# Optimization experiments

Measured on AMD Instinct MI355X. Metric: run time of the kernel, lower is better.

Reference implementation:

```python
import jax, jax.numpy as jnp
import numpy as np

D_MODEL = 1024
N_HEADS = 16
HEAD = D_MODEL // N_HEADS
B, S = 2, 2048


def setup_inputs() -> dict:
    key = jax.random.key(0)
    ks = jax.random.split(key, 9)
    sc = 1.0 / np.sqrt(D_MODEL)
    return {
        "q": jax.random.normal(ks[0], (B, S, D_MODEL), dtype=jnp.float32),
        "k": jax.random.normal(ks[1], (B, S, D_MODEL), dtype=jnp.float32),
        "v": jax.random.normal(ks[2], (B, S, D_MODEL), dtype=jnp.float32),
        "mask": jnp.zeros((S, S), dtype=jnp.float32),
        "Wq": jax.random.normal(ks[3], (D_MODEL, D_MODEL), dtype=jnp.float32) * sc,
        "bq": jnp.zeros((D_MODEL,), dtype=jnp.float32),
        "Wk": jax.random.normal(ks[4], (D_MODEL, D_MODEL), dtype=jnp.float32) * sc,
        "bk": jnp.zeros((D_MODEL,), dtype=jnp.float32),
        "Wv": jax.random.normal(ks[5], (D_MODEL, D_MODEL), dtype=jnp.float32) * sc,
        "bv": jnpp_zeros() if False else jnp.zeros((D_MODEL,), dtype=jnp.float32),
    }


def reference(q, k, v, mask, Wq, bq, Wk, bk, Wv, bv):
    # Linear projections (torch Linear: x @ W.T + b)
    qp = q @ Wq.T + bq  # (B, S, D)
    kp = k @ Wk.T + bk
    vp = v @ Wv.T + bv
    # split heads -> (B, H, S, Hd)
    def split(x):
        return x.reshape(B, S, N_HEADS, HEAD).transpose(0, 2, 1, 3)
    qh, kh, vh = split(qp), split(kp), split(vp)
    scores = jnp.einsum('bhqd,bhkd->bhqk', qh, kh) / np.sqrt(HEAD)
    scores = scores + mask  # additive mask broadcast over (B, H)
    attn = jax.nn.softmax(scores, axis=-1)
    out = jnp.einsum('bhqk,bhkd->bhqd', attn, vh)
    return out.transpose(0, 2, 1, 3).reshape(B, S, D_MODEL)
```

## Files before the change

### kernel.cpp

```cpp
#include <hip/hip_runtime.h>
#include <cstdint>

#define DM 1024
#define NH 16
#define HDIM 64
#define SEQ 2048
#define NB 2
#define L2E 1.44269504f

typedef unsigned short u16;
typedef unsigned int u32;
typedef __attribute__((ext_vector_type(8))) short bf16x8;
typedef __attribute__((ext_vector_type(8))) unsigned short u16x8;
typedef __attribute__((ext_vector_type(4))) unsigned int u32x4;
typedef __attribute__((ext_vector_type(4))) float f32x4;
typedef __attribute__((ext_vector_type(16))) float f32x16;
typedef __attribute__((ext_vector_type(4))) unsigned short u16x4;

__device__ __forceinline__ u16 f2bf(float f) {
  uint32_t x = __float_as_uint(f);
  x += 0x7fffu + ((x >> 16) & 1u);
  return (u16)(x >> 16);
}

__device__ __forceinline__ u32 pack_bf2t(float lo, float hi) {
  return __builtin_amdgcn_perm(__float_as_uint(hi), __float_as_uint(lo), 0x07060302u);
}

__device__ __forceinline__ void gload_lds16(const void* g, void* lds) {
  __builtin_amdgcn_global_load_lds(
      (const __attribute__((address_space(1))) unsigned int*)(uintptr_t)g,
      (__attribute__((address_space(3))) unsigned int*)(uint32_t)(uintptr_t)lds,
      16, 0, 0);
}


__global__ __launch_bounds__(256) void prep_kernel(
    const float4* __restrict__ W0, const float4* __restrict__ W1, const float4* __restrict__ W2,
    u16x4* __restrict__ d0, u16x4* __restrict__ d1, u16x4* __restrict__ d2,
    const float* __restrict__ mask, u16* __restrict__ maskP) {
  const int bx = blockIdx.x;
  const int t = threadIdx.x;
  if (bx < 3072) {
    const int i = bx * 256 + t;
    const int seg = i >> 18, off = i & 262143;
    const float4* s = seg == 0 ? W0 : (seg == 1 ? W1 : W2);
    u16x4* d = seg == 0 ? d0 : (seg == 1 ? d1 : d2);
    float4 v = s[off];
    u16x4 o = {f2bf(v.x), f2bf(v.y), f2bf(v.z), f2bf(v.w)};
    d[off] = o;
    return;
  }
  __shared__ float tile[32][257];
  const int mb = bx - 3072;
  const int q0 = (mb & 63) * 32;
  const int yt = mb >> 6;
#pragma unroll
  for (int ss = 0; ss < 2; ++ss) {
    const int st = yt * 2 + ss;
    const int kv0 = st * 256;
    if (ss) __syncthreads();
#pragma unroll
    for (int p = 0; p < 8; ++p) {
      const int row = p * 4 + (t >> 6);
      const int col = (t & 63) * 4;
      *(float4*)&tile[row][col] = *(const float4*)&mask[(size_t)(q0 + row) * SEQ + kv0 + col];
    }
    __syncthreads();
    const int tgl = t >> 5, ql = t & 31;
    u16 outv[32];
#pragma unroll
    for (int i = 0; i < 32; ++i) {
      const int hl = i >> 4, r = i & 15;
      const int kvl = (r & 3) + 8 * (r >> 2) + 4 * hl;
      outv[i] = f2bf(tile[ql][tgl * 32 + kvl] * L2E);
    }
    u16* dst = maskP + ((size_t)(st * 8 + tgl) * SEQ + (q0 + ql)) * 32;
#pragma unroll
    for (int j = 0; j < 4; ++j) *(u16x8*)(dst + 8 * j) = *(const u16x8*)&outv[8 * j];
  }
}

__global__ __launch_bounds__(256) void proj_kernel(
    const float* __restrict__ Xq, const float* __restrict__ Xk, const float* __restrict__ Xv,
    const u16* __restrict__ Wqp, const u16* __restrict__ Wkp, const u16* __restrict__ Wvp,
    const float* __restrict__ bqp, const float* __restrict__ bkp, const float* __restrict__ bvp,
    u16* __restrict__ Qp, u16* __restrict__ Kp, u16* __restrict__ Vt) {
  __shared__ __align__(16) u16 sA[2][128 * 32];
  __shared__ __align__(16) u16 sB[2][128 * 32];
  const int t = threadIdx.x;
  const int w = t >> 6, lane = t & 63, quad = lane >> 4, l16 = lane & 15;
  const int wr = w >> 1, wc = w & 1;
  const int m0 = blockIdx.y * 128, n0 = blockIdx.x * 128;
  const int mode = blockIdx.z;
  const float* X = mode == 0 ? Xq : (mode == 1 ? Xk : Xv);
  const u16* W = mode == 0 ? Wqp : (mode == 1 ? Wkp : Wvp);
  const float* bias = mode == 0 ? bqp : (mode == 1 ? bkp : bvp);

  f32x4 acc[4][4] = {};
  const int ar = t >> 3;
  const int ac = t & 7;
  const int srow = lane >> 2;
  const int scol = (lane & 3) * 16;

  {
    float4 x0[4];
#pragma unroll
    for (int rr = 0; rr < 4; ++rr)
      x0[rr] = *(const float4*)&X[(size_t)(m0 + rr * 32 + ar) * DM + ac * 4];
#pragma unroll
    for (int rr = 0; rr < 4; ++rr) {
      u16x4 pk = {f2bf(x0[rr].x), f2bf(x0[rr].y), f2bf(x0[rr].z), f2bf(x0[rr].w)};
      *(u16x4*)&sA[0][(rr * 32 + ar) * 32 + ac * 4] = pk;
    }
#pragma unroll
    for (int j = 0; j < 2; ++j) {
      const int rbase = (w * 2 + j) * 16;
      gload_lds16((const char*)W + ((size_t)(n0 + rbase + srow) * DM) * 2 + scol,
                  (char*)sB[0] + rbase * 64);
    }
  }

  for (int it = 0; it < 32; ++it) {
    const int p = it & 1;
    __syncthreads();
    float4 xn[4];
    if (it < 31) {
      const int k0 = (it + 1) * 32;
#pragma unroll
      for (int rr = 0; rr < 4; ++rr)
        xn[rr] = *(const float4*)&X[(size_t)(m0 + rr * 32 + ar) * DM + k0 + ac * 4];
#pragma unroll
      for (int j = 0; j < 2; ++j) {
        const int rbase = (w * 2 + j) * 16;
        gload_lds16((const char*)W + ((size_t)(n0 + rbase + srow) * DM + k0) * 2 + scol,
                    (char*)sB[p ^ 1] + rbase * 64);
      }
    }
    bf16x8 af[4], bfr[4];
#pragma unroll
    for (int i = 0; i < 4; ++i)
      af[i] = *(const bf16x8*)&sA[p][(wr * 64 + i * 16 + l16) * 32 + quad * 8];
#pragma unroll
    for (int j = 0; j < 4; ++j)
      bfr[j] = *(const bf16x8*)&sB[p][(wc * 64 + j * 16 + l16) * 32 + quad * 8];
#pragma unroll
    for (int i = 0; i < 4; ++i)
#pragma unroll
      for (int j = 0; j < 4; ++j)
        acc[i][j] = __builtin_amdgcn_mfma_f32_16x16x32_bf16(af[i], bfr[j], acc[i][j], 0, 0, 0);
    if (it < 31) {
#pragma unroll
      for (int rr = 0; rr < 4; ++rr) {
        u16x4 pk = {f2bf(xn[rr].x), f2bf(xn[rr].y), f2bf(xn[rr].z), f2bf(xn[rr].w)};
        *(u16x4*)&sA[p ^ 1][(rr * 32 + ar) * 32 + ac * 4] = pk;
      }
    }
  }

  float bb[4];
#pragma unroll
  for (int j = 0; j < 4; ++j) bb[j] = bias[n0 + wc * 64 + j * 16 + l16];
  const float scl = (mode == 0) ? 0.18033688011f : 1.0f;

#pragma unroll
  for (int i = 0; i < 4; ++i) {
    const int mbase = m0 + wr * 64 + i * 16 + quad * 4;
    const int bidx = mbase >> 11;
    const int s = mbase & 2047;
#pragma unroll
    for (int j = 0; j < 4; ++j) {
      const int n = n0 + wc * 64 + j * 16 + l16;
      const int h = n >> 6, hd = n & 63;
      const size_t hb = (size_t)(bidx * NH + h) * (SEQ * HDIM);
      if (mode == 2) {
        const int tv = (s >> 5) * 2048 + (hd >> 5) * 1024 + ((s >> 4) & 1) * 512 +
                       ((s >> 3) & 1) * 256 + (hd & 31) * 8 + (s & 7);
        u16x4 pk = {f2bf(acc[i][j][0] + bb[j]), f2bf(acc[i][j][1] + bb[j]),
                    f2bf(acc[i][j][2] + bb[j]), f2bf(acc[i][j][3] + bb[j])};
        *(u16x4*)&Vt[hb + tv] = pk;
      } else {
        u16* dst = (mode == 0) ? Qp : Kp;
        const int th = (s >> 5) * 2048 + (hd >> 4) * 512 + ((hd >> 3) & 1) * 256 +
                       (s & 31) * 8 + (hd & 7);
#pragma unroll
        for (int r = 0; r < 4; ++r)
          dst[hb + th + r * 8] = f2bf((acc[i][j][r] + bb[j]) * scl);
      }
    }
  }
}

__global__ __launch_bounds__(128, 2) void attn_kernel(
    const u16* __restrict__ Qp, const u16* __restrict__ Kp,
    const u16* __restrict__ Vt, const u16* __restrict__ maskP,
    float* __restrict__ out) {
  __shared__ float sO[2][32][65];
  __shared__ float sL[2][64];
  const int t = threadIdx.x, w = t >> 6, lane = t & 63;
  const int l31 = lane & 31, hl = lane >> 5;
  const int h = blockIdx.x, qt = blockIdx.y, b = blockIdx.z;
  const int q0 = qt * 64;
  const u16* Qh = Qp + (size_t)(b * NH + h) * (SEQ * HDIM);
  const u16* Kh = Kp + (size_t)(b * NH + h) * (SEQ * HDIM);
  const u16* Vh = Vt + (size_t)(b * NH + h) * (SEQ * HDIM);

  bf16x8 qf[2][4];
#pragma unroll
  for (int sub = 0; sub < 2; ++sub)
#pragma unroll
    for (int kt = 0; kt < 4; ++kt)
      qf[sub][kt] =
          *(const bf16x8*)(Qh + (size_t)((q0 >> 5) + sub) * 2048 + kt * 512 + lane * 8);

  const int Tb = w * 32;
  const u16* Kt = Kh + (size_t)Tb * 2048 + (size_t)lane * 8;
  const u16* Vw = Vh + (size_t)Tb * 2048 + (size_t)lane * 8;
  const u16* mb0 = maskP + ((size_t)Tb * SEQ + (q0 + l31)) * 32 + hl * 16;
  const u16* mb1 = mb0 + 32 * 32;

  f32x16 oacc[2][2] = {};
  float l_run[2] = {0.f, 0.f};

  bf16x8 kf[4];
#pragma unroll
  for (int kt = 0; kt < 4; ++kt) kf[kt] = *(const bf16x8*)(Kt + kt * 512);
  u32x4 mk[2][2];
  mk[0][0] = *(const u32x4*)(mb0);
  mk[0][1] = *(const u32x4*)(mb0 + 8);
  mk[1][0] = *(const u32x4*)(mb1);
  mk[1][1] = *(const u32x4*)(mb1 + 8);

#pragma unroll 2
  for (int it = 0; it < 32; ++it) {
    bf16x8 vf[2][2];
#pragma unroll
    for (int half = 0; half < 2; ++half)
#pragma unroll
      for (int ks = 0; ks < 2; ++ks)
        vf[half][ks] =
            *(const bf16x8*)(Vw + (size_t)it * 2048 + half * 1024 + ks * 512);

    const int itn = it < 31 ? it + 1 : 31;
    bf16x8 kfn[4];
#pragma unroll
    for (int kt = 0; kt < 4; ++kt)
      kfn[kt] = *(const bf16x8*)(Kt + (size_t)itn * 2048 + kt * 512);
    u32x4 mkn[2][2];
    mkn[0][0] = *(const u32x4*)(mb0 + (size_t)itn * (SEQ * 32));
    mkn[0][1] = *(const u32x4*)(mb0 + (size_t)itn * (SEQ * 32) + 8);
    mkn[1][0] = *(const u32x4*)(mb1 + (size_t)itn * (SEQ * 32));
    mkn[1][1] = *(const u32x4*)(mb1 + (size_t)itn * (SEQ * 32) + 8);

    bf16x8 pfr[2][2];
#pragma unroll
    for (int sub = 0; sub < 2; ++sub) {
      f32x16 st;
#pragma unroll
      for (int r = 0; r < 8; ++r) {
        const u32 word = (r < 4 ? mk[sub][0][r & 3] : mk[sub][1][r & 3]);
        st[2 * r] = __uint_as_float(word << 16);
        st[2 * r + 1] = __uint_as_float(word & 0xffff0000u);
      }
#pragma unroll
      for (int kt = 0; kt < 4; ++kt)
        st = __builtin_amdgcn_mfma_f32_32x32x16_bf16(kf[kt], qf[sub][kt], st, 0, 0, 0);

      float ls = 0.f;
#pragma unroll
      for (int r = 0; r < 16; ++r) {
        st[r] = __builtin_amdgcn_exp2f(st[r]);
        ls += st[r];
      }
      l_run[sub] += ls;

      u32 pk[4][2];
#pragma unroll
      for (int g = 0; g < 4; ++g) {
        pk[g][0] = pack_bf2t(st[4 * g + 0], st[4 * g + 1]);
        pk[g][1] = pack_bf2t(st[4 * g + 2], st[4 * g + 3]);
      }
#pragma unroll
      for (int ks = 0; ks < 2; ++ks) {
        u32 sa = hl ? pk[2 * ks][0] : pk[2 * ks + 1][0];
        u32 sb = hl ? pk[2 * ks][1] : pk[2 * ks + 1][1];
        u32 ra = __shfl_xor(sa, 32);
        u32 rb = __shfl_xor(sb, 32);
        u32 oa = hl ? pk[2 * ks + 1][0] : pk[2 * ks][0];
        u32 ob = hl ? pk[2 * ks + 1][1] : pk[2 * ks][1];
        union {
          u32 u[4];
          bf16x8 v;
        } f;
        f.u[0] = hl ? ra : oa;
        f.u[1] = hl ? rb : ob;
        f.u[2] = hl ? oa : ra;
        f.u[3] = hl ? ob : rb;
        pfr[sub][ks] = f.v;
      }
    }

#pragma unroll
    for (int sub = 0; sub < 2; ++sub)
#pragma unroll
      for (int ks = 0; ks < 2; ++ks) {
        oacc[0][sub] = __builtin_amdgcn_mfma_f32_32x32x16_bf16(vf[0][ks], pfr[sub][ks],
                                                               oacc[0][sub], 0, 0, 0);
        oacc[1][sub] = __builtin_amdgcn_mfma_f32_32x32x16_bf16(vf[1][ks], pfr[sub][ks],
                                                               oacc[1][sub], 0, 0, 0);
      }

#pragma unroll
    for (int kt = 0; kt < 4; ++kt) kf[kt] = kfn[kt];
#pragma unroll
    for (int sub = 0; sub < 2; ++sub) {
      mk[sub][0] = mkn[sub][0];
      mk[sub][1] = mkn[sub][1];
    }
  }

  l_run[0] += __shfl_xor(l_run[0], 32);
  l_run[1] += __shfl_xor(l_run[1], 32);
  if (hl == 0) {
    sL[w][l31] = l_run[0];
    sL[w][32 + l31] = l_run[1];
  }

  const int hd = t & 31, grp = t >> 5;
#pragma unroll
  for (int half = 0; half < 2; ++half) {
    __syncthreads();
#pragma unroll
    for (int sub = 0; sub < 2; ++sub)
#pragma unroll
      for (int r = 0; r < 16; ++r)
        sO[w][(r & 3) + 8 * (r >> 2) + 4 * hl][sub * 32 + l31] = oacc[half][sub][r];
    __syncthreads();
#pragma unroll
    for (int p16 = 0; p16 < 16; ++p16) {
      const int qi = grp * 16 + p16;
      const float lsum = sL[0][qi] + sL[1][qi];
      const float val = sO[0][hd][qi] + sO[1][hd][qi];
      out[(size_t)(b * SEQ + q0 + qi) * DM + h * HDIM + half * 32 + hd] = val / lsum;
    }
  }
}

extern "C" void kernel_launch(void* const* d_in, const int* in_sizes, int n_in,
                              void* d_out, int out_size, void* d_ws, size_t ws_size,
                              hipStream_t stream) {
  const float* q = (const float*)d_in[0];
  const float* k = (const float*)d_in[1];
  const float* v = (const float*)d_in[2];
  const float* mask = (const float*)d_in[3];
  const float* Wq = (const float*)d_in[4];
  const float* bq = (const float*)d_in[5];
  const float* Wk = (const float*)d_in[6];
  const float* bk = (const float*)d_in[7];
  const float* Wv = (const float*)d_in[8];
  const float* bv = (const float*)d_in[9];

  char* ws = (char*)d_ws;
  u16* wq_bf = (u16*)(ws + 0);
  u16* wk_bf = (u16*)(ws + 2097152);
  u16* wv_bf = (u16*)(ws + 4194304);
  u16* Qp = (u16*)(ws + 6291456);
  u16* Kp = (u16*)(ws + 14680064);
  u16* Vt = (u16*)(ws + 23068672);
  u16* maskP = (u16*)(ws + 31457280);

  prep_kernel<<<3328, 256, 0, stream>>>((const float4*)Wq, (const float4*)Wk,
                                        (const float4*)Wv, (u16x4*)wq_bf, (u16x4*)wk_bf,
                                        (u16x4*)wv_bf, mask, maskP);

  proj_kernel<<<dim3(8, 32, 3), 256, 0, stream>>>(q, k, v, wq_bf, wk_bf, wv_bf,
                                                  bq, bk, bv, Qp, Kp, Vt);

  attn_kernel<<<dim3(16, 32, 2), 128, 0, stream>>>(Qp, Kp, Vt, maskP, (float*)d_out);
}
```

Before: 227.6 us.

## Remap blocks across XCDs for L2 locality, store mask as fp32, vectorize X staging

The proj and attention grids are flattened to 1D and block indices are remapped so that blocks sharing the same head or row tile land on the same XCD (L & 7), which should improve per-XCD L2 reuse of K/V and weights. The pre-permuted mask is now kept in fp32 instead of bf16, which removes the unpack step in the attention loop and keeps full mask precision, but doubles mask traffic. The X tile staging in proj is reorganized so each lane writes 8 bf16 values with a single 16-byte LDS store. The fp32 mask also doubles the workspace footprint of that buffer.

```diff
diff --git a/kernel.cpp b/kernel.cpp
--- a/kernel.cpp
+++ b/kernel.cpp
@@ -38,7 +38,7 @@
 __global__ __launch_bounds__(256) void prep_kernel(
     const float4* __restrict__ W0, const float4* __restrict__ W1, const float4* __restrict__ W2,
     u16x4* __restrict__ d0, u16x4* __restrict__ d1, u16x4* __restrict__ d2,
-    const float* __restrict__ mask, u16* __restrict__ maskP) {
+    const float* __restrict__ mask, float* __restrict__ maskPf) {
   const int bx = blockIdx.x;
   const int t = threadIdx.x;
   if (bx < 3072) {
@@ -68,16 +68,16 @@
     }
     __syncthreads();
     const int tgl = t >> 5, ql = t & 31;
-    u16 outv[32];
+    float outv[32];
 #pragma unroll
     for (int i = 0; i < 32; ++i) {
       const int hl = i >> 4, r = i & 15;
       const int kvl = (r & 3) + 8 * (r >> 2) + 4 * hl;
-      outv[i] = f2bf(tile[ql][tgl * 32 + kvl] * L2E);
-    }
-    u16* dst = maskP + ((size_t)(st * 8 + tgl) * SEQ + (q0 + ql)) * 32;
-#pragma unroll
-    for (int j = 0; j < 4; ++j) *(u16x8*)(dst + 8 * j) = *(const u16x8*)&outv[8 * j];
+      outv[i] = tile[ql][tgl * 32 + kvl] * L2E;
+    }
+    float* dst = maskPf + ((size_t)(st * 8 + tgl) * SEQ + (q0 + ql)) * 32;
+#pragma unroll
+    for (int j = 0; j < 8; ++j) *(float4*)(dst + 4 * j) = *(const float4*)&outv[4 * j];
   }
 }
 
@@ -91,27 +91,37 @@
   const int t = threadIdx.x;
   const int w = t >> 6, lane = t & 63, quad = lane >> 4, l16 = lane & 15;
   const int wr = w >> 1, wc = w & 1;
-  const int m0 = blockIdx.y * 128, n0 = blockIdx.x * 128;
-  const int mode = blockIdx.z;
+  const int L = blockIdx.x;
+  const int xcd = L & 7;
+  const int p5 = L >> 3;
+  const int n_t = p5 & 7;
+  const int g = xcd + 8 * (p5 >> 3);
+  const int mode = g >> 5;
+  const int m_t = g & 31;
+  const int m0 = m_t * 128, n0 = n_t * 128;
   const float* X = mode == 0 ? Xq : (mode == 1 ? Xk : Xv);
   const u16* W = mode == 0 ? Wqp : (mode == 1 ? Wkp : Wvp);
   const float* bias = mode == 0 ? bqp : (mode == 1 ? bkp : bvp);
 
   f32x4 acc[4][4] = {};
-  const int ar = t >> 3;
-  const int ac = t & 7;
+  const int arow = lane >> 2;
+  const int acol = lane & 3;
   const int srow = lane >> 2;
   const int scol = (lane & 3) * 16;
 
   {
-    float4 x0[4];
-#pragma unroll
-    for (int rr = 0; rr < 4; ++rr)
-      x0[rr] = *(const float4*)&X[(size_t)(m0 + rr * 32 + ar) * DM + ac * 4];
-#pragma unroll
-    for (int rr = 0; rr < 4; ++rr) {
-      u16x4 pk = {f2bf(x0[rr].x), f2bf(x0[rr].y), f2bf(x0[rr].z), f2bf(x0[rr].w)};
-      *(u16x4*)&sA[0][(rr * 32 + ar) * 32 + ac * 4] = pk;
+    float4 xa[2][2];
+#pragma unroll
+    for (int j = 0; j < 2; ++j) {
+      const int r = w * 32 + j * 16 + arow;
+      xa[j][0] = *(const float4*)&X[(size_t)(m0 + r) * DM + acol * 8];
+      xa[j][1] = *(const float4*)&X[(size_t)(m0 + r) * DM + acol * 8 + 4];
+    }
+#pragma unroll
+    for (int j = 0; j < 2; ++j) {
+      u16x8 pk = {f2bf(xa[j][0].x), f2bf(xa[j][0].y), f2bf(xa[j][0].z), f2bf(xa[j][0].w),
+                  f2bf(xa[j][1].x), f2bf(xa[j][1].y), f2bf(xa[j][1].z), f2bf(xa[j][1].w)};
+      *(u16x8*)&sA[0][(w * 32 + j * 16) * 32 + lane * 8] = pk;
     }
 #pragma unroll
     for (int j = 0; j < 2; ++j) {
@@ -124,12 +134,15 @@
   for (int it = 0; it < 32; ++it) {
     const int p = it & 1;
     __syncthreads();
-    float4 xn[4];
+    float4 xn[2][2];
     if (it < 31) {
       const int k0 = (it + 1) * 32;
 #pragma unroll
-      for (int rr = 0; rr < 4; ++rr)
-        xn[rr] = *(const float4*)&X[(size_t)(m0 + rr * 32 + ar) * DM + k0 + ac * 4];
+      for (int j = 0; j < 2; ++j) {
+        const int r = w * 32 + j * 16 + arow;
+        xn[j][0] = *(const float4*)&X[(size_t)(m0 + r) * DM + k0 + acol * 8];
+        xn[j][1] = *(const float4*)&X[(size_t)(m0 + r) * DM + k0 + acol * 8 + 4];
+      }
 #pragma unroll
       for (int j = 0; j < 2; ++j) {
         const int rbase = (w * 2 + j) * 16;
@@ -151,9 +164,10 @@
         acc[i][j] = __builtin_amdgcn_mfma_f32_16x16x32_bf16(af[i], bfr[j], acc[i][j], 0, 0, 0);
     if (it < 31) {
 #pragma unroll
-      for (int rr = 0; rr < 4; ++rr) {
-        u16x4 pk = {f2bf(xn[rr].x), f2bf(xn[rr].y), f2bf(xn[rr].z), f2bf(xn[rr].w)};
-        *(u16x4*)&sA[p ^ 1][(rr * 32 + ar) * 32 + ac * 4] = pk;
+      for (int j = 0; j < 2; ++j) {
+        u16x8 pk = {f2bf(xn[j][0].x), f2bf(xn[j][0].y), f2bf(xn[j][0].z), f2bf(xn[j][0].w),
+                    f2bf(xn[j][1].x), f2bf(xn[j][1].y), f2bf(xn[j][1].z), f2bf(xn[j][1].w)};
+        *(u16x8*)&sA[p ^ 1][(w * 32 + j * 16) * 32 + lane * 8] = pk;
       }
     }
   }
@@ -193,13 +207,18 @@
 
 __global__ __launch_bounds__(128, 2) void attn_kernel(
     const u16* __restrict__ Qp, const u16* __restrict__ Kp,
-    const u16* __restrict__ Vt, const u16* __restrict__ maskP,
+    const u16* __restrict__ Vt, const float* __restrict__ maskPf,
     float* __restrict__ out) {
   __shared__ float sO[2][32][65];
   __shared__ float sL[2][64];
   const int t = threadIdx.x, w = t >> 6, lane = t & 63;
   const int l31 = lane & 31, hl = lane >> 5;
-  const int h = blockIdx.x, qt = blockIdx.y, b = blockIdx.z;
+  const int L = blockIdx.x;
+  const int xcd = L & 7;
+  const int idx = L >> 3;
+  const int qt = idx & 31;
+  const int bh = xcd + 8 * (idx >> 5);
+  const int h = bh & 15, b = bh >> 4;
   const int q0 = qt * 64;
   const u16* Qh = Qp + (size_t)(b * NH + h) * (SEQ * HDIM);
   const u16* Kh = Kp + (size_t)(b * NH + h) * (SEQ * HDIM);
@@ -216,8 +235,8 @@
   const int Tb = w * 32;
   const u16* Kt = Kh + (size_t)Tb * 2048 + (size_t)lane * 8;
   const u16* Vw = Vh + (size_t)Tb * 2048 + (size_t)lane * 8;
-  const u16* mb0 = maskP + ((size_t)Tb * SEQ + (q0 + l31)) * 32 + hl * 16;
-  const u16* mb1 = mb0 + 32 * 32;
+  const float* mb0 = maskPf + ((size_t)Tb * SEQ + (q0 + l31)) * 32 + hl * 16;
+  const float* mb1 = mb0 + 32 * 32;
 
   f32x16 oacc[2][2] = {};
   float l_run[2] = {0.f, 0.f};
@@ -225,11 +244,12 @@
   bf16x8 kf[4];
 #pragma unroll
   for (int kt = 0; kt < 4; ++kt) kf[kt] = *(const bf16x8*)(Kt + kt * 512);
-  u32x4 mk[2][2];
-  mk[0][0] = *(const u32x4*)(mb0);
-  mk[0][1] = *(const u32x4*)(mb0 + 8);
-  mk[1][0] = *(const u32x4*)(mb1);
-  mk[1][1] = *(const u32x4*)(mb1 + 8);
+  f32x4 mk[2][4];
+#pragma unroll
+  for (int sub = 0; sub < 2; ++sub)
+#pragma unroll
+    for (int g = 0; g < 4; ++g)
+      mk[sub][g] = *(const f32x4*)((sub ? mb1 : mb0) + 4 * g);
 
 #pragma unroll 2
   for (int it = 0; it < 32; ++it) {
@@ -246,22 +266,19 @@
 #pragma unroll
     for (int kt = 0; kt < 4; ++kt)
       kfn[kt] = *(const bf16x8*)(Kt + (size_t)itn * 2048 + kt * 512);
-    u32x4 mkn[2][2];
-    mkn[0][0] = *(const u32x4*)(mb0 + (size_t)itn * (SEQ * 32));
-    mkn[0][1] = *(const u32x4*)(mb0 + (size_t)itn * (SEQ * 32) + 8);
-    mkn[1][0] = *(const u32x4*)(mb1 + (size_t)itn * (SEQ * 32));
-    mkn[1][1] = *(const u32x4*)(mb1 + (size_t)itn * (SEQ * 32) + 8);
+    f32x4 mkn[2][4];
+#pragma unroll
+    for (int sub = 0; sub < 2; ++sub)
+#pragma unroll
+      for (int g = 0; g < 4; ++g)
+        mkn[sub][g] = *(const f32x4*)((sub ? mb1 : mb0) + (size_t)itn * (SEQ * 32) + 4 * g);
 
     bf16x8 pfr[2][2];
 #pragma unroll
     for (int sub = 0; sub < 2; ++sub) {
       f32x16 st;
 #pragma unroll
-      for (int r = 0; r < 8; ++r) {
-        const u32 word = (r < 4 ? mk[sub][0][r & 3] : mk[sub][1][r & 3]);
-        st[2 * r] = __uint_as_float(word << 16);
-        st[2 * r + 1] = __uint_as_float(word & 0xffff0000u);
-      }
+      for (int r = 0; r < 16; ++r) st[r] = mk[sub][r >> 2][r & 3];
 #pragma unroll
       for (int kt = 0; kt < 4; ++kt)
         st = __builtin_amdgcn_mfma_f32_32x32x16_bf16(kf[kt], qf[sub][kt], st, 0, 0, 0);
@@ -313,10 +330,9 @@
 #pragma unroll
     for (int kt = 0; kt < 4; ++kt) kf[kt] = kfn[kt];
 #pragma unroll
-    for (int sub = 0; sub < 2; ++sub) {
-      mk[sub][0] = mkn[sub][0];
-      mk[sub][1] = mkn[sub][1];
-    }
+    for (int sub = 0; sub < 2; ++sub)
+#pragma unroll
+      for (int g = 0; g < 4; ++g) mk[sub][g] = mkn[sub][g];
   }
 
   l_run[0] += __shfl_xor(l_run[0], 32);
@@ -367,14 +383,14 @@
   u16* Qp = (u16*)(ws + 6291456);
   u16* Kp = (u16*)(ws + 14680064);
   u16* Vt = (u16*)(ws + 23068672);
-  u16* maskP = (u16*)(ws + 31457280);
+  float* maskPf = (float*)(ws + 31457280);
 
   prep_kernel<<<3328, 256, 0, stream>>>((const float4*)Wq, (const float4*)Wk,
                                         (const float4*)Wv, (u16x4*)wq_bf, (u16x4*)wk_bf,
-                                        (u16x4*)wv_bf, mask, maskP);
-
-  proj_kernel<<<dim3(8, 32, 3), 256, 0, stream>>>(q, k, v, wq_bf, wk_bf, wv_bf,
-                                                  bq, bk, bv, Qp, Kp, Vt);
-
-  attn_kernel<<<dim3(16, 32, 2), 128, 0, stream>>>(Qp, Kp, Vt, maskP, (float*)d_out);
-}
+                                        (u16x4*)wv_bf, mask, maskPf);
+
+  proj_kernel<<<768, 256, 0, stream>>>(q, k, v, wq_bf, wk_bf, wv_bf,
+                                       bq, bk, bv, Qp, Kp, Vt);
+
+  attn_kernel<<<1024, 128, 0, stream>>>(Qp, Kp, Vt, maskPf, (float*)d_out);
+}
```

Result: slower. 274.7 us (+20.7%).
